# Kernel tuning notes

Measured on AMD Instinct MI355X. Metric: run time of the kernel, lower is better.

Reference implementation:

```python
import jax, jax.numpy as jnp
import numpy as np
from jax import lax

B, GRID = 256, 58  # 28*2+2 per scn.InputLayer spatial size


def _conv(x, w):
    # x: [B,C,H,W], w: [O,C,k,k]; scn.Convolution is VALID, stride 1, no bias
    return lax.conv_general_dilated(
        x, w, window_strides=(1, 1), padding='VALID',
        dimension_numbers=('NCHW', 'OIHW', 'NCHW'))


def _maxpool2(x):
    return lax.reduce_window(x, -jnp.inf, lax.max,
                             window_dimensions=(1, 1, 2, 2),
                             window_strides=(1, 1, 2, 2), padding='VALID')


def setup_inputs() -> dict:
    key = jax.random.key(0)
    k0, k1, k2, k3, k4 = jax.random.split(key, 5)
    return {
        'x': jax.random.normal(k0, (B, 1, GRID, GRID), dtype=jnp.float32),
        'w1': jax.random.normal(k1, (64, 1, 5, 5), dtype=jnp.float32) * 0.1,
        'w2': jax.random.normal(k2, (128, 64, 5, 5), dtype=jnp.float32) * 0.025,
        'lw': jax.random.normal(k3, (10, 128), dtype=jnp.float32) * 0.09,
        'lb': jax.random.normal(k4, (10,), dtype=jnp.float32) * 0.01,
    }


def reference(x, w1, w2, lw, lb):
    h = _conv(x, w1)          # [B,64,54,54]
    h = _maxpool2(h)          # [B,64,27,27]
    h = _conv(h, w2)          # [B,128,23,23]
    h = jnp.transpose(h, (0, 2, 3, 1))  # channels-last for linear
    return jnp.einsum('bhwc,oc->bhwo', h, lw) + lb  # [B,23,23,10]
```

## Files before the change

### kernel.cpp

```cpp
#include <hip/hip_runtime.h>


typedef __attribute__((ext_vector_type(8))) short bf16x8;
typedef __attribute__((ext_vector_type(4))) float f32x4;
typedef __attribute__((ext_vector_type(4))) unsigned int u32x4;

#define MFMA16(a, b, c) __builtin_amdgcn_mfma_f32_16x16x32_bf16((a), (b), (c), 0, 0, 0)

static __device__ __forceinline__ unsigned short f2bf(float f) {
    unsigned u = __builtin_bit_cast(unsigned, f);
    u += 0x7FFFu + ((u >> 16) & 1u);
    return (unsigned short)(u >> 16);
}

__global__ __launch_bounds__(256) void prep_w2c(
    const float* __restrict__ w2, unsigned short* __restrict__ w2c)
{
    int t = blockIdx.x * 256 + threadIdx.x;
    if (t >= 25600) return;
    const int lane = t & 63, khalf = (t >> 6) & 1, nt = (t >> 7) & 7, kk = t >> 10;
    const int l16 = lane & 15, kg = lane >> 4;
    const int oc = nt * 16 + l16;
    const int icb = khalf * 32 + kg * 8;
    unsigned pk[4];
#pragma unroll
    for (int h = 0; h < 4; ++h) {
        unsigned short lo = f2bf(w2[oc * 1600 + (icb + 2 * h) * 25 + kk]);
        unsigned short hi = f2bf(w2[oc * 1600 + (icb + 2 * h + 1) * 25 + kk]);
        pk[h] = (unsigned)lo | ((unsigned)hi << 16);
    }
    u32x4 v; v.x = pk[0]; v.y = pk[1]; v.z = pk[2]; v.w = pk[3];
    *(u32x4*)(w2c + (size_t)t * 8) = v;
}

#define XBF_OFF  104976
#define W1T_OFF  111704
#define ECON_STR 272
#define LWT_OFF  147968
#define LDS_TOT  152320

__global__ __launch_bounds__(512, 2) void fused_net(
    const float* __restrict__ x, const float* __restrict__ w1,
    const unsigned short* __restrict__ w2c,
    const float* __restrict__ lw, const float* __restrict__ lb,
    float* __restrict__ out)
{
    extern __shared__ char lds[];
    unsigned short* xbf = (unsigned short*)(lds + XBF_OFF);
    unsigned short* w1t = (unsigned short*)(lds + W1T_OFF);
    const int b = blockIdx.x, tid = threadIdx.x;
    const int lane = tid & 63, w = tid >> 6;
    const int l16 = lane & 15, kg = lane >> 4;

    const float4* xg = (const float4*)(x + b * 3364);
    for (int i = tid; i < 841; i += 512) {
        float4 v = xg[i];
        unsigned p0 = (unsigned)f2bf(v.x) | ((unsigned)f2bf(v.y) << 16);
        unsigned p1 = (unsigned)f2bf(v.z) | ((unsigned)f2bf(v.w) << 16);
        *(uint2*)(xbf + i * 4) = make_uint2(p0, p1);
    }
    for (int i = tid; i < 2048; i += 512) {
        int k = i >> 6, oc = i & 63;
        w1t[i] = (k < 25) ? f2bf(w1[oc * 25 + k]) : (unsigned short)0;
    }
    for (int i = tid; i < 2048; i += 512) {
        int o = i >> 7, cc = i & 127;
        float v = (o < 10) ? lw[o * 128 + cc] : 0.f;
        *(unsigned short*)(lds + LWT_OFF + o * 272 + cc * 2) = f2bf(v);
    }
    __syncthreads();

    {
        int koff[8];
        unsigned kmsk[8];
#pragma unroll
        for (int j = 0; j < 8; ++j) {
            int k = kg * 8 + j;
            int kh = k / 5, kw = k - 5 * kh;
            koff[j] = (k < 25) ? (kh * 58 + kw) : 0;
            kmsk[j] = (k < 25) ? 0xFFFFu : 0u;
        }
        bf16x8 bfrag[4];
#pragma unroll
        for (int ot = 0; ot < 4; ++ot)
#pragma unroll
            for (int j = 0; j < 8; ++j)
                bfrag[ot][j] = (short)w1t[(kg * 8 + j) * 64 + ot * 16 + l16];

        const f32x4 zero4 = {0.f, 0.f, 0.f, 0.f};
        for (int t = w; t < 183; t += 8) {
            int p = t * 4 + (l16 >> 2);
            if (p > 728) p = 728;
            const int q = l16 & 3;
            const int ph = p / 27, pw = p - 27 * ph;
            const int base = (2 * ph + (q >> 1)) * 58 + 2 * pw + (q & 1);
            bf16x8 afrag;
#pragma unroll
            for (int j = 0; j < 8; ++j)
                afrag[j] = (short)(xbf[base + koff[j]] & kmsk[j]);
            f32x4 acc1[4];
#pragma unroll
            for (int ot = 0; ot < 4; ++ot)
                acc1[ot] = MFMA16(afrag, bfrag[ot], zero4);
            const int pout = t * 4 + kg;
            if (pout < 729) {
#pragma unroll
                for (int ot = 0; ot < 4; ++ot) {
                    float m = fmaxf(fmaxf(acc1[ot][0], acc1[ot][1]),
                                    fmaxf(acc1[ot][2], acc1[ot][3]));
                    *(unsigned short*)(lds + pout * 144 + (ot * 16 + l16) * 2)
                        = f2bf(m);
                }
            }
        }
    }
    __syncthreads();

    const int mtc = (w < 2) ? 5 : 4;
    int abase[5];
#pragma unroll
    for (int ti = 0; ti < 5; ++ti) {
        int tile = w + 8 * ti;
        if (tile > 33) tile = w;
        const int tstart = (tile == 33) ? 513 : tile * 16;
        const int sp = tstart + l16;
        const int oh = sp / 23, ow = sp - oh * 23;
        abase[ti] = (oh * 27 + ow) * 144 + kg * 16;
    }

    f32x4 acc[5][8];
#pragma unroll
    for (int ti = 0; ti < 5; ++ti)
#pragma unroll
        for (int nt = 0; nt < 8; ++nt)
            acc[ti][nt] = (f32x4){0.f, 0.f, 0.f, 0.f};

    for (int kk = 0; kk < 25; ++kk) {
        const int kh = kk / 5, kw = kk - 5 * kh;
        const int pixoffB = (kh * 27 + kw) * 144;
        const unsigned short* wp = w2c + (size_t)kk * 8192 + lane * 8;
#pragma unroll
        for (int hf = 0; hf < 2; ++hf) {
            bf16x8 Bf[8];
#pragma unroll
            for (int nt = 0; nt < 8; ++nt)
                Bf[nt] = *(const bf16x8*)(wp + (nt * 2 + hf) * 512);
#pragma unroll
            for (int ti = 0; ti < 5; ++ti) {
                if (ti < mtc) {
                    bf16x8 a =
                        *(const bf16x8*)(lds + abase[ti] + pixoffB + hf * 64);
#pragma unroll
                    for (int nt = 0; nt < 8; ++nt)
                        acc[ti][nt] = MFMA16(a, Bf[nt], acc[ti][nt]);
                }
            }
        }
    }

    __syncthreads();
#pragma unroll
    for (int ti = 0; ti < 5; ++ti) {
        if (ti < mtc) {
            int tile = w + 8 * ti;
            if (tile > 33) tile = w;
            const int rbase = ((tile == 33) ? 513 : tile * 16) + kg * 4;
#pragma unroll
            for (int nt = 0; nt < 8; ++nt) {
                const int col = nt * 16 + l16;
#pragma unroll
                for (int r = 0; r < 4; ++r)
                    *(unsigned short*)(lds + (rbase + r) * ECON_STR + col * 2)
                        = f2bf(acc[ti][nt][r]);
            }
        }
    }
    __syncthreads();

    const float lbv = (l16 < 10) ? lb[l16] : 0.f;
#pragma unroll
    for (int i = 0; i < 5; ++i) {
        const int t = w + 8 * i;
        if (t < 34) {
            f32x4 al = {0.f, 0.f, 0.f, 0.f};
            const char* arow = lds + (t * 16 + l16) * ECON_STR + kg * 16;
            const char* brow = lds + LWT_OFF + l16 * 272 + kg * 16;
#pragma unroll
            for (int ks = 0; ks < 4; ++ks) {
                bf16x8 av = *(const bf16x8*)(arow + ks * 64);
                bf16x8 bv = *(const bf16x8*)(brow + ks * 64);
                al = MFMA16(av, bv, al);
            }
            if (l16 < 10) {
#pragma unroll
                for (int r = 0; r < 4; ++r) {
                    int sp = t * 16 + kg * 4 + r;
                    if (sp < 529)
                        out[((size_t)b * 529 + sp) * 10 + l16] = al[r] + lbv;
                }
            }
        }
    }
}

extern "C" void kernel_launch(void* const* d_in, const int* in_sizes, int n_in,
                              void* d_out, int out_size, void* d_ws, size_t ws_size,
                              hipStream_t stream) {
    const float* x  = (const float*)d_in[0];
    const float* w1 = (const float*)d_in[1];
    const float* w2 = (const float*)d_in[2];
    const float* lw = (const float*)d_in[3];
    const float* lb = (const float*)d_in[4];
    float* out = (float*)d_out;

    unsigned short* w2c = (unsigned short*)d_ws;

    (void)hipFuncSetAttribute((const void*)fused_net,
                              hipFuncAttributeMaxDynamicSharedMemorySize,
                              LDS_TOT);

    prep_w2c<<<100, 256, 0, stream>>>(w2, w2c);
    fused_net<<<256, 512, LDS_TOT, stream>>>(x, w1, w2c, lw, lb, out);
}
```

Measured before the change: 66.04 us.

## Switch conv2 to 32x32x16 MFMA with 4x2 wave tiling and narrower LDS stride

Conv2 now uses 32x32x16 bf16 MFMA tiles. The eight waves split into four M-groups (output pixel tiles of 32) and two N-groups (64 output channels each), and the weight prep kernel repacks w2 to match. The pooled activation row stride shrinks from 144 to 136 bytes to change LDS bank mapping, so A fragments are now loaded as two 8-byte reads. The aim is fewer MFMA issues and fewer global weight loads per wave, since each wave fetches only its half of the output channels. In exchange the accumulators grow larger, which adds register pressure, and the unaligned split loads add LDS instructions.

```diff
diff --git a/kernel.cpp b/kernel.cpp
--- a/kernel.cpp
+++ b/kernel.cpp
@@ -3,9 +3,12 @@
 
 typedef __attribute__((ext_vector_type(8))) short bf16x8;
 typedef __attribute__((ext_vector_type(4))) float f32x4;
+typedef __attribute__((ext_vector_type(16))) float f32x16;
+typedef __attribute__((ext_vector_type(2))) unsigned int u32x2;
 typedef __attribute__((ext_vector_type(4))) unsigned int u32x4;
 
 #define MFMA16(a, b, c) __builtin_amdgcn_mfma_f32_16x16x32_bf16((a), (b), (c), 0, 0, 0)
+#define MFMA32(a, b, c) __builtin_amdgcn_mfma_f32_32x32x16_bf16((a), (b), (c), 0, 0, 0)
 
 static __device__ __forceinline__ unsigned short f2bf(float f) {
     unsigned u = __builtin_bit_cast(unsigned, f);
@@ -13,35 +16,35 @@
     return (unsigned short)(u >> 16);
 }
 
-__global__ __launch_bounds__(256) void prep_w2c(
-    const float* __restrict__ w2, unsigned short* __restrict__ w2c)
+__global__ __launch_bounds__(256) void prep_w2d(
+    const float* __restrict__ w2, unsigned short* __restrict__ w2d)
 {
     int t = blockIdx.x * 256 + threadIdx.x;
     if (t >= 25600) return;
-    const int lane = t & 63, khalf = (t >> 6) & 1, nt = (t >> 7) & 7, kk = t >> 10;
-    const int l16 = lane & 15, kg = lane >> 4;
-    const int oc = nt * 16 + l16;
-    const int icb = khalf * 32 + kg * 8;
+    const int lane = t & 63, nt = (t >> 6) & 3, ks = (t >> 8) & 3, kk = t >> 10;
+    const int oc = nt * 32 + (lane & 31);
+    const int ic0 = ks * 16 + (lane >> 5) * 8;
     unsigned pk[4];
 #pragma unroll
     for (int h = 0; h < 4; ++h) {
-        unsigned short lo = f2bf(w2[oc * 1600 + (icb + 2 * h) * 25 + kk]);
-        unsigned short hi = f2bf(w2[oc * 1600 + (icb + 2 * h + 1) * 25 + kk]);
+        unsigned short lo = f2bf(w2[oc * 1600 + (ic0 + 2 * h) * 25 + kk]);
+        unsigned short hi = f2bf(w2[oc * 1600 + (ic0 + 2 * h + 1) * 25 + kk]);
         pk[h] = (unsigned)lo | ((unsigned)hi << 16);
     }
     u32x4 v; v.x = pk[0]; v.y = pk[1]; v.z = pk[2]; v.w = pk[3];
-    *(u32x4*)(w2c + (size_t)t * 8) = v;
-}
-
-#define XBF_OFF  104976
-#define W1T_OFF  111704
+    *(u32x4*)(w2d + (size_t)t * 8) = v;
+}
+
+#define XS_STR   136
+#define XBF_OFF  99144
+#define W1T_OFF  105872
 #define ECON_STR 272
 #define LWT_OFF  147968
 #define LDS_TOT  152320
 
 __global__ __launch_bounds__(512, 2) void fused_net(
     const float* __restrict__ x, const float* __restrict__ w1,
-    const unsigned short* __restrict__ w2c,
+    const unsigned short* __restrict__ w2d,
     const float* __restrict__ lw, const float* __restrict__ lb,
     float* __restrict__ out)
 {
@@ -51,6 +54,8 @@
     const int b = blockIdx.x, tid = threadIdx.x;
     const int lane = tid & 63, w = tid >> 6;
     const int l16 = lane & 15, kg = lane >> 4;
+    const int l32 = lane & 31, kg2 = lane >> 5;
+    const int mgrp = w >> 1, ngrp = w & 1;
 
     const float4* xg = (const float4*)(x + b * 3364);
     for (int i = tid; i < 841; i += 512) {
@@ -108,7 +113,7 @@
                 for (int ot = 0; ot < 4; ++ot) {
                     float m = fmaxf(fmaxf(acc1[ot][0], acc1[ot][1]),
                                     fmaxf(acc1[ot][2], acc1[ot][3]));
-                    *(unsigned short*)(lds + pout * 144 + (ot * 16 + l16) * 2)
+                    *(unsigned short*)(lds + pout * XS_STR + (ot * 16 + l16) * 2)
                         = f2bf(m);
                 }
             }
@@ -116,62 +121,69 @@
     }
     __syncthreads();
 
-    const int mtc = (w < 2) ? 5 : 4;
-    int abase[5];
-#pragma unroll
-    for (int ti = 0; ti < 5; ++ti) {
-        int tile = w + 8 * ti;
-        if (tile > 33) tile = w;
-        const int tstart = (tile == 33) ? 513 : tile * 16;
-        const int sp = tstart + l16;
+    const int mcnt = (mgrp == 0) ? 5 : 4;
+    int ts[5], abase[5];
+#pragma unroll
+    for (int i = 0; i < 5; ++i) {
+        int tile = (mgrp == 0) ? i : 5 + (mgrp - 1) * 4 + i;
+        if (i >= mcnt) tile = mgrp;
+        int tstart = tile * 32;
+        if (tstart > 497) tstart = 497;
+        ts[i] = tstart;
+        const int sp = tstart + l32;
         const int oh = sp / 23, ow = sp - oh * 23;
-        abase[ti] = (oh * 27 + ow) * 144 + kg * 16;
-    }
-
-    f32x4 acc[5][8];
-#pragma unroll
-    for (int ti = 0; ti < 5; ++ti)
-#pragma unroll
-        for (int nt = 0; nt < 8; ++nt)
-            acc[ti][nt] = (f32x4){0.f, 0.f, 0.f, 0.f};
+        abase[i] = (oh * 27 + ow) * XS_STR + kg2 * 16;
+    }
+
+    f32x16 acc[5][2];
+#pragma unroll
+    for (int i = 0; i < 5; ++i)
+#pragma unroll
+        for (int j = 0; j < 2; ++j)
+#pragma unroll
+            for (int r = 0; r < 16; ++r) acc[i][j][r] = 0.f;
 
     for (int kk = 0; kk < 25; ++kk) {
         const int kh = kk / 5, kw = kk - 5 * kh;
-        const int pixoffB = (kh * 27 + kw) * 144;
-        const unsigned short* wp = w2c + (size_t)kk * 8192 + lane * 8;
-#pragma unroll
-        for (int hf = 0; hf < 2; ++hf) {
-            bf16x8 Bf[8];
-#pragma unroll
-            for (int nt = 0; nt < 8; ++nt)
-                Bf[nt] = *(const bf16x8*)(wp + (nt * 2 + hf) * 512);
-#pragma unroll
-            for (int ti = 0; ti < 5; ++ti) {
-                if (ti < mtc) {
-                    bf16x8 a =
-                        *(const bf16x8*)(lds + abase[ti] + pixoffB + hf * 64);
-#pragma unroll
-                    for (int nt = 0; nt < 8; ++nt)
-                        acc[ti][nt] = MFMA16(a, Bf[nt], acc[ti][nt]);
-                }
-            }
-        }
-    }
-
-    __syncthreads();
-#pragma unroll
-    for (int ti = 0; ti < 5; ++ti) {
-        if (ti < mtc) {
-            int tile = w + 8 * ti;
-            if (tile > 33) tile = w;
-            const int rbase = ((tile == 33) ? 513 : tile * 16) + kg * 4;
-#pragma unroll
-            for (int nt = 0; nt < 8; ++nt) {
-                const int col = nt * 16 + l16;
-#pragma unroll
-                for (int r = 0; r < 4; ++r)
-                    *(unsigned short*)(lds + (rbase + r) * ECON_STR + col * 2)
-                        = f2bf(acc[ti][nt][r]);
+        const int pixoff = (kh * 27 + kw) * XS_STR;
+        bf16x8 Bf[4][2];
+#pragma unroll
+        for (int ks = 0; ks < 4; ++ks)
+#pragma unroll
+            for (int j = 0; j < 2; ++j)
+                Bf[ks][j] = *(const bf16x8*)(
+                    w2d + ((size_t)kk * 1024 + ks * 256 +
+                           (ngrp * 2 + j) * 64 + lane) * 8);
+#pragma unroll
+        for (int ks = 0; ks < 4; ++ks) {
+#pragma unroll
+            for (int i = 0; i < 5; ++i) {
+                if (i < mcnt) {
+                    const char* ap = lds + abase[i] + pixoff + ks * 32;
+                    u32x2 lo = *(const u32x2*)(ap);
+                    u32x2 hi = *(const u32x2*)(ap + 8);
+                    u32x4 t4; t4.x = lo.x; t4.y = lo.y; t4.z = hi.x; t4.w = hi.y;
+                    bf16x8 a = __builtin_bit_cast(bf16x8, t4);
+                    acc[i][0] = MFMA32(a, Bf[ks][0], acc[i][0]);
+                    acc[i][1] = MFMA32(a, Bf[ks][1], acc[i][1]);
+                }
+            }
+        }
+    }
+
+    __syncthreads();
+#pragma unroll
+    for (int i = 0; i < 5; ++i) {
+        if (i < mcnt) {
+#pragma unroll
+            for (int j = 0; j < 2; ++j) {
+                const int col = (ngrp * 2 + j) * 32 + l32;
+#pragma unroll
+                for (int reg = 0; reg < 16; ++reg) {
+                    const int row = (reg & 3) + 8 * (reg >> 2) + 4 * kg2;
+                    *(unsigned short*)(lds + (ts[i] + row) * ECON_STR + col * 2)
+                        = f2bf(acc[i][j][reg]);
+                }
             }
         }
     }
@@ -213,12 +225,12 @@
     const float* lb = (const float*)d_in[4];
     float* out = (float*)d_out;
 
-    unsigned short* w2c = (unsigned short*)d_ws;
+    unsigned short* w2d = (unsigned short*)d_ws;
 
     (void)hipFuncSetAttribute((const void*)fused_net,
                               hipFuncAttributeMaxDynamicSharedMemorySize,
                               LDS_TOT);
 
-    prep_w2c<<<100, 256, 0, stream>>>(w2, w2c);
-    fused_net<<<256, 512, LDS_TOT, stream>>>(x, w1, w2c, lw, lb, out);
-}
+    prep_w2d<<<100, 256, 0, stream>>>(w2, w2d);
+    fused_net<<<256, 512, LDS_TOT, stream>>>(x, w1, w2d, lw, lb, out);
+}
```

New measurement: 71.75 us. +8.7%, slower.

## Double-buffer conv2 weight fragments, stagger kernel offsets per wave, add setprio

Applied to the files above, without the earlier changes.

Conv2's main loop now keeps two register buffers of weight fragments, so the global loads for the next half-step are issued while MFMAs run on the current buffer. Half of the waves start at kernel offset 12 and wrap around, which spreads their global and L2 accesses over different weight slices. s_setprio raises wave priority around the MFMA bursts. The extra buffer adds register pressure on a kernel already holding 160 accumulator registers at launch bounds 512,2, so spills or lower occupancy are a risk.

```diff
diff --git a/kernel.cpp b/kernel.cpp
--- a/kernel.cpp
+++ b/kernel.cpp
@@ -18,10 +18,10 @@
 {
     int t = blockIdx.x * 256 + threadIdx.x;
     if (t >= 25600) return;
-    const int lane = t & 63, khalf = (t >> 6) & 1, nt = (t >> 7) & 7, kk = t >> 10;
+    const int lane = t & 63, hf = (t >> 6) & 1, nt = (t >> 7) & 7, kk = t >> 10;
     const int l16 = lane & 15, kg = lane >> 4;
     const int oc = nt * 16 + l16;
-    const int icb = khalf * 32 + kg * 8;
+    const int icb = hf * 32 + kg * 8;
     unsigned pk[4];
 #pragma unroll
     for (int h = 0; h < 4; ++h) {
@@ -135,27 +135,43 @@
         for (int nt = 0; nt < 8; ++nt)
             acc[ti][nt] = (f32x4){0.f, 0.f, 0.f, 0.f};
 
+    auto loadBhf = [&](bf16x8* dst, int kkv, int hf) {
+        const unsigned short* p =
+            w2c + (size_t)kkv * 8192 + hf * 512 + lane * 8;
+#pragma unroll
+        for (int nt = 0; nt < 8; ++nt)
+            dst[nt] = *(const bf16x8*)(p + nt * 1024);
+    };
+    auto computeHF = [&](int kkv, int hf, const bf16x8* B) {
+        const int kh = kkv / 5, kw = kkv - 5 * kh;
+        const int pixoff = (kh * 27 + kw) * 144 + hf * 64;
+#pragma unroll
+        for (int ti = 0; ti < 5; ++ti) {
+            if (ti < mtc) {
+                bf16x8 a = *(const bf16x8*)(lds + abase[ti] + pixoff);
+#pragma unroll
+                for (int nt = 0; nt < 8; ++nt)
+                    acc[ti][nt] = MFMA16(a, B[nt], acc[ti][nt]);
+            }
+        }
+    };
+
+    const int koffs = ((w >> 2) & 1) * 12;
+    bf16x8 BA[8], BB[8];
+    int kcur = koffs;
+    loadBhf(BA, kcur, 0);
     for (int kk = 0; kk < 25; ++kk) {
-        const int kh = kk / 5, kw = kk - 5 * kh;
-        const int pixoffB = (kh * 27 + kw) * 144;
-        const unsigned short* wp = w2c + (size_t)kk * 8192 + lane * 8;
-#pragma unroll
-        for (int hf = 0; hf < 2; ++hf) {
-            bf16x8 Bf[8];
-#pragma unroll
-            for (int nt = 0; nt < 8; ++nt)
-                Bf[nt] = *(const bf16x8*)(wp + (nt * 2 + hf) * 512);
-#pragma unroll
-            for (int ti = 0; ti < 5; ++ti) {
-                if (ti < mtc) {
-                    bf16x8 a =
-                        *(const bf16x8*)(lds + abase[ti] + pixoffB + hf * 64);
-#pragma unroll
-                    for (int nt = 0; nt < 8; ++nt)
-                        acc[ti][nt] = MFMA16(a, Bf[nt], acc[ti][nt]);
-                }
-            }
-        }
+        int knxt = kcur + 1;
+        if (knxt >= 25) knxt -= 25;
+        loadBhf(BB, kcur, 1);
+        __builtin_amdgcn_s_setprio(1);
+        computeHF(kcur, 0, BA);
+        __builtin_amdgcn_s_setprio(0);
+        if (kk + 1 < 25) loadBhf(BA, knxt, 0);
+        __builtin_amdgcn_s_setprio(1);
+        computeHF(kcur, 1, BB);
+        __builtin_amdgcn_s_setprio(0);
+        kcur = knxt;
     }
 
     __syncthreads();
```

After: 77.44 us. +17.3%, slower.

## Double block to 1024 threads, splitting conv2 output channels across wave pairs

Applied to the files above, without the earlier changes.

Raises the fused kernel to 1024 threads (16 waves) per block. In conv2 each pair of waves shares the same spatial tiles and splits the 128 output channels into two halves, which halves the accumulator registers per wave. Conv1 and the linear stage are spread over the extra waves. LDS use (~152KB) still allows only one block per CU, so latency hiding comes only from more waves per block. Each A fragment is now loaded from LDS by two waves, and the launch_bounds(1024,4) hint may constrain registers.

```diff
diff --git a/kernel.cpp b/kernel.cpp
--- a/kernel.cpp
+++ b/kernel.cpp
@@ -18,10 +18,10 @@
 {
     int t = blockIdx.x * 256 + threadIdx.x;
     if (t >= 25600) return;
-    const int lane = t & 63, khalf = (t >> 6) & 1, nt = (t >> 7) & 7, kk = t >> 10;
+    const int lane = t & 63, hf = (t >> 6) & 1, nt = (t >> 7) & 7, kk = t >> 10;
     const int l16 = lane & 15, kg = lane >> 4;
     const int oc = nt * 16 + l16;
-    const int icb = khalf * 32 + kg * 8;
+    const int icb = hf * 32 + kg * 8;
     unsigned pk[4];
 #pragma unroll
     for (int h = 0; h < 4; ++h) {
@@ -39,7 +39,7 @@
 #define LWT_OFF  147968
 #define LDS_TOT  152320
 
-__global__ __launch_bounds__(512, 2) void fused_net(
+__global__ __launch_bounds__(1024, 4) void fused_net(
     const float* __restrict__ x, const float* __restrict__ w1,
     const unsigned short* __restrict__ w2c,
     const float* __restrict__ lw, const float* __restrict__ lb,
@@ -51,19 +51,20 @@
     const int b = blockIdx.x, tid = threadIdx.x;
     const int lane = tid & 63, w = tid >> 6;
     const int l16 = lane & 15, kg = lane >> 4;
+    const int mgrp = w >> 1, ngrp = w & 1;
 
     const float4* xg = (const float4*)(x + b * 3364);
-    for (int i = tid; i < 841; i += 512) {
+    for (int i = tid; i < 841; i += 1024) {
         float4 v = xg[i];
         unsigned p0 = (unsigned)f2bf(v.x) | ((unsigned)f2bf(v.y) << 16);
         unsigned p1 = (unsigned)f2bf(v.z) | ((unsigned)f2bf(v.w) << 16);
         *(uint2*)(xbf + i * 4) = make_uint2(p0, p1);
     }
-    for (int i = tid; i < 2048; i += 512) {
+    for (int i = tid; i < 2048; i += 1024) {
         int k = i >> 6, oc = i & 63;
         w1t[i] = (k < 25) ? f2bf(w1[oc * 25 + k]) : (unsigned short)0;
     }
-    for (int i = tid; i < 2048; i += 512) {
+    for (int i = tid; i < 2048; i += 1024) {
         int o = i >> 7, cc = i & 127;
         float v = (o < 10) ? lw[o * 128 + cc] : 0.f;
         *(unsigned short*)(lds + LWT_OFF + o * 272 + cc * 2) = f2bf(v);
@@ -88,7 +89,7 @@
                 bfrag[ot][j] = (short)w1t[(kg * 8 + j) * 64 + ot * 16 + l16];
 
         const f32x4 zero4 = {0.f, 0.f, 0.f, 0.f};
-        for (int t = w; t < 183; t += 8) {
+        for (int t = w; t < 183; t += 16) {
             int p = t * 4 + (l16 >> 2);
             if (p > 728) p = 728;
             const int q = l16 & 3;
@@ -116,43 +117,44 @@
     }
     __syncthreads();
 
-    const int mtc = (w < 2) ? 5 : 4;
+    const int mtc = (mgrp < 2) ? 5 : 4;
     int abase[5];
 #pragma unroll
     for (int ti = 0; ti < 5; ++ti) {
-        int tile = w + 8 * ti;
-        if (tile > 33) tile = w;
+        int tile = mgrp + 8 * ti;
+        if (tile > 33) tile = mgrp;
         const int tstart = (tile == 33) ? 513 : tile * 16;
         const int sp = tstart + l16;
         const int oh = sp / 23, ow = sp - oh * 23;
         abase[ti] = (oh * 27 + ow) * 144 + kg * 16;
     }
 
-    f32x4 acc[5][8];
+    f32x4 acc[5][4];
 #pragma unroll
     for (int ti = 0; ti < 5; ++ti)
 #pragma unroll
-        for (int nt = 0; nt < 8; ++nt)
+        for (int nt = 0; nt < 4; ++nt)
             acc[ti][nt] = (f32x4){0.f, 0.f, 0.f, 0.f};
 
     for (int kk = 0; kk < 25; ++kk) {
         const int kh = kk / 5, kw = kk - 5 * kh;
-        const int pixoffB = (kh * 27 + kw) * 144;
-        const unsigned short* wp = w2c + (size_t)kk * 8192 + lane * 8;
+        const int pixoff = (kh * 27 + kw) * 144;
+        const unsigned short* wp =
+            w2c + (size_t)kk * 8192 + (ngrp * 4) * 1024 + lane * 8;
 #pragma unroll
         for (int hf = 0; hf < 2; ++hf) {
-            bf16x8 Bf[8];
-#pragma unroll
-            for (int nt = 0; nt < 8; ++nt)
-                Bf[nt] = *(const bf16x8*)(wp + (nt * 2 + hf) * 512);
+            bf16x8 Bf[4];
+#pragma unroll
+            for (int j = 0; j < 4; ++j)
+                Bf[j] = *(const bf16x8*)(wp + j * 1024 + hf * 512);
 #pragma unroll
             for (int ti = 0; ti < 5; ++ti) {
                 if (ti < mtc) {
                     bf16x8 a =
-                        *(const bf16x8*)(lds + abase[ti] + pixoffB + hf * 64);
-#pragma unroll
-                    for (int nt = 0; nt < 8; ++nt)
-                        acc[ti][nt] = MFMA16(a, Bf[nt], acc[ti][nt]);
+                        *(const bf16x8*)(lds + abase[ti] + pixoff + hf * 64);
+#pragma unroll
+                    for (int j = 0; j < 4; ++j)
+                        acc[ti][j] = MFMA16(a, Bf[j], acc[ti][j]);
                 }
             }
         }
@@ -162,16 +164,16 @@
 #pragma unroll
     for (int ti = 0; ti < 5; ++ti) {
         if (ti < mtc) {
-            int tile = w + 8 * ti;
-            if (tile > 33) tile = w;
+            int tile = mgrp + 8 * ti;
+            if (tile > 33) tile = mgrp;
             const int rbase = ((tile == 33) ? 513 : tile * 16) + kg * 4;
 #pragma unroll
-            for (int nt = 0; nt < 8; ++nt) {
-                const int col = nt * 16 + l16;
+            for (int j = 0; j < 4; ++j) {
+                const int col = (ngrp * 4 + j) * 16 + l16;
 #pragma unroll
                 for (int r = 0; r < 4; ++r)
                     *(unsigned short*)(lds + (rbase + r) * ECON_STR + col * 2)
-                        = f2bf(acc[ti][nt][r]);
+                        = f2bf(acc[ti][j][r]);
             }
         }
     }
@@ -179,8 +181,8 @@
 
     const float lbv = (l16 < 10) ? lb[l16] : 0.f;
 #pragma unroll
-    for (int i = 0; i < 5; ++i) {
-        const int t = w + 8 * i;
+    for (int i = 0; i < 3; ++i) {
+        const int t = w + 16 * i;
         if (t < 34) {
             f32x4 al = {0.f, 0.f, 0.f, 0.f};
             const char* arow = lds + (t * 16 + l16) * ECON_STR + kg * 16;
@@ -220,5 +222,5 @@
                               LDS_TOT);
 
     prep_w2c<<<100, 256, 0, stream>>>(w2, w2c);
-    fused_net<<<256, 512, LDS_TOT, stream>>>(x, w1, w2c, lw, lb, out);
-}
+    fused_net<<<256, 1024, LDS_TOT, stream>>>(x, w1, w2c, lw, lb, out);
+}
```

Result: no change. 66.79 us (+1.1%).
